# Kernel tuning notes

Measured on AMD Instinct MI355X. Metric: run time of the kernel, lower is better.

## Reference

```python
import jax, jax.numpy as jnp
import numpy as np

B, Q, C, G = 16, 2000, 80, 100
COST_CLASS, COST_BBOX, COST_GIOU = 2.0, 5.0, 2.0
ALPHA, GAMMA = 0.25, 2.0
OTA_K = 5
CENTER_RADIUS = 2.5
MAX_ITERS = 1000  # safety cap on the (normally rarely-entered) rescue while-loop


def cxcywh_to_xyxy(b):
    cx, cy, w, h = jnp.split(b, 4, axis=-1)
    return jnp.concatenate([cx - 0.5 * w, cy - 0.5 * h, cx + 0.5 * w, cy + 0.5 * h], -1)


def xyxy_to_cxcywh(b):
    x1, y1, x2, y2 = jnp.split(b, 4, axis=-1)
    return jnp.concatenate([(x1 + x2) * 0.5, (y1 + y2) * 0.5, x2 - x1, y2 - y1], -1)


def box_iou(a, b):
    # a: [Q,4], b: [G,4] xyxy -> iou [Q,G], union [Q,G]
    area_a = (a[:, 2] - a[:, 0]) * (a[:, 3] - a[:, 1])
    area_b = (b[:, 2] - b[:, 0]) * (b[:, 3] - b[:, 1])
    lt = jnp.maximum(a[:, None, :2], b[None, :, :2])
    rb = jnp.minimum(a[:, None, 2:], b[None, :, 2:])
    wh = jnp.clip(rb - lt, 0.0)
    inter = wh[..., 0] * wh[..., 1]
    union = area_a[:, None] + area_b[None, :] - inter
    return inter / union, union


def generalized_box_iou(a, b):
    iou, union = box_iou(a, b)
    lt = jnp.minimum(a[:, None, :2], b[None, :, :2])
    rb = jnp.maximum(a[:, None, 2:], b[None, :, 2:])
    wh = jnp.clip(rb - lt, 0.0)
    area = wh[..., 0] * wh[..., 1]
    return iou - (area - union) / area


def get_in_boxes_info(boxes_c, tgt_c):
    # boxes_c: [Q,4] cxcywh (abs), tgt_c: [G,4] cxcywh (abs)
    xy = cxcywh_to_xyxy(tgt_c)  # [G,4]
    ax = boxes_c[:, 0:1]  # [Q,1]
    ay = boxes_c[:, 1:2]
    in_box = (ax > xy[:, 0][None, :]) & (ax < xy[:, 2][None, :]) & \
             (ay > xy[:, 1][None, :]) & (ay < xy[:, 3][None, :])  # [Q,G]
    w = xy[:, 2] - xy[:, 0]
    h = xy[:, 3] - xy[:, 1]
    in_ctr = (ax > (tgt_c[:, 0] - CENTER_RADIUS * w)[None, :]) & \
             (ax < (tgt_c[:, 0] + CENTER_RADIUS * w)[None, :]) & \
             (ay > (tgt_c[:, 1] - CENTER_RADIUS * h)[None, :]) & \
             (ay < (tgt_c[:, 1] + CENTER_RADIUS * h)[None, :])
    fg_mask = in_box.any(1) | in_ctr.any(1)  # [Q]
    return fg_mask, in_box & in_ctr


def dynamic_k_matching(cost, ious):
    # cost, ious: [Q,G]
    topk_ious, _ = jax.lax.top_k(ious.T, OTA_K)  # [G,k]
    dyn_k = jnp.clip(topk_ious.sum(1).astype(jnp.int32), 1, None)  # [G], <= OTA_K
    # rank of each query within each gt column (ascending cost, stable ties)
    ranks = jnp.argsort(jnp.argsort(cost, axis=0), axis=0)
    M = (ranks < dyn_k[None, :]).astype(cost.dtype)  # topk(largest=False) per column

    onehot = lambda idx: jax.nn.one_hot(idx, G, dtype=cost.dtype)
    # resolve anchors matched to >1 gt: keep the min-cost gt
    conflict0 = M.sum(1) > 1  # stale mask reused inside the while loop (faithful to torch code)
    M = jnp.where(conflict0[:, None], onehot(jnp.argmin(cost, axis=1)), M)

    qidx = jnp.arange(Q)

    def cond(state):
        M, cost, it = state
        return ((M.sum(0) == 0).any()) & (it < MAX_ITERS)

    def body(state):
        M, cost, it = state
        matched = M.sum(1) > 0
        cost = cost + 100000.0 * matched[:, None].astype(cost.dtype)
        unmatched_gt = M.sum(0) == 0  # [G]
        pos = jnp.argmin(cost, axis=0)  # [G] best anchor per gt (same cost for all, as in torch)
        add = unmatched_gt[None, :] & (qidx[:, None] == pos[None, :])
        M = jnp.where(add, jnp.asarray(1.0, cost.dtype), M)
        has_conf = (M.sum(1) > 1).any()
        M = jnp.where((has_conf & conflict0)[:, None], onehot(jnp.argmin(cost, axis=1)), M)
        return M, cost, it + 1

    M, cost, _ = jax.lax.while_loop(cond, body, (M, cost, jnp.int32(0)))

    selected = M.sum(1) > 0  # [Q] bool
    gt_idx = jnp.argmax(M, axis=1).astype(jnp.int32)  # [Q] (valid where selected)
    cost_m = jnp.where(M == 0, jnp.asarray(1e30, cost.dtype), cost)
    matched_qid = jnp.argmin(cost_m, axis=0).astype(jnp.int32)  # [G]
    return selected, gt_idx, matched_qid, M


def _match_one(logits, boxes, gtb, labels, img):
    # logits [Q,C], boxes [Q,4] cxcywh, gtb [G,4] cxcywh norm, labels [G] int, img [4]
    prob = jax.nn.sigmoid(logits)
    boxes_abs = cxcywh_to_xyxy(boxes) * img
    gt_abs = cxcywh_to_xyxy(gtb) * img
    fg_mask, in_bc = get_in_boxes_info(xyxy_to_cxcywh(boxes_abs), xyxy_to_cxcywh(gt_abs))
    ious, _ = box_iou(boxes_abs, gt_abs)
    neg = (1.0 - ALPHA) * prob ** GAMMA * (-jnp.log(1.0 - prob + 1e-8))
    pos = ALPHA * (1.0 - prob) ** GAMMA * (-jnp.log(prob + 1e-8))
    cost_class = (pos - neg)[:, labels]  # [Q,G]
    cost_bbox = jnp.sum(jnp.abs(boxes_abs[:, None, :] / img - gt_abs[None, :, :] / img), -1)
    cost_giou = -generalized_box_iou(boxes_abs, gt_abs)
    cost = (COST_BBOX * cost_bbox + COST_CLASS * cost_class + COST_GIOU * cost_giou
            + 100.0 * (~in_bc).astype(cost_bbox.dtype)
            + 10000.0 * (~fg_mask)[:, None].astype(cost_bbox.dtype))
    return dynamic_k_matching(cost, ious)


def setup_inputs() -> dict:
    key = jax.random.key(0)
    k1, k2, k3, k4 = jax.random.split(key, 4)
    return {
        "pred_logits": jax.random.normal(k1, (B, Q, C), dtype=jnp.float32),
        "pred_boxes": jax.random.uniform(k2, (B, Q, 4), dtype=jnp.float32),
        "gt_boxes": jax.random.uniform(k3, (B, G, 4), dtype=jnp.float32),
        "labels": jax.random.randint(k4, (B, G), 0, C),
        "image_size_xyxy": jnp.ones((B, 4), dtype=jnp.float32),
    }


def reference(pred_logits, pred_boxes, gt_boxes, labels, image_size_xyxy):
    selected, gt_idx, matched_qid, M = jax.vmap(_match_one)(
        pred_logits, pred_boxes, gt_boxes, labels, image_size_xyxy)
    # selected [B,Q] bool, gt_idx [B,Q] int32, matched_qid [B,G] int32, M [B,Q,G] float
    return selected, gt_idx, matched_qid, M
```

## Files before the change

### kernel.cpp

```cpp
#include <hip/hip_runtime.h>
#include <stdint.h>

#define BATCH 16
#define NQ 2000
#define NC 80
#define NG 100
#define MAX_ITERS 1000
#define MAXC 96
#define QT 32
#define TILES 63
#define K1_TILEB (BATCH * TILES)
#define K1_BLOCKS (K1_TILEB + 400)
#define K3_BS 1024
#define NW3 16
#define NCAND 8
#define LSTRIDE 9
#define QINF 0x7fffffff
#define SQINF 0x7fff

#define OFF_SEL 0
#define OFF_GTI (BATCH * NQ)
#define OFF_MQ (2 * BATCH * NQ)
#define OFF_M (2 * BATCH * NQ + BATCH * NG)

#define WS_COST  0
#define WS_LISTS 12800000
#define WS_MW    12864000
#define WS_MIT   13376000
#define WS_CIDX  13440000
#define WS_CROW  13504000
#define WS_SCAL  14118400
#define WS_NEED  14118912

__device__ __forceinline__ float fmut(float c, int k) {
    for (int i = 0; i < k; ++i) c += 100000.0f;
    return c;
}

__device__ __forceinline__ bool lexlt(float v1, int i1, float v2, int i2) {
    return (v1 < v2) | ((v1 == v2) & (i1 < i2));
}

#define CE(vv, ii, a, b) do { \
    bool t_ = lexlt(vv[b], ii[b], vv[a], ii[a]); \
    float lo_ = t_ ? vv[b] : vv[a]; float hi_ = t_ ? vv[a] : vv[b]; \
    int loi_ = t_ ? ii[b] : ii[a]; int hii_ = t_ ? ii[a] : ii[b]; \
    vv[a] = lo_; vv[b] = hi_; ii[a] = loi_; ii[b] = hii_; \
} while (0)

#define INS8(vv, ii, val, idx) do { float v_ = (val); int i_ = (idx); \
    bool ins_ = lexlt(v_, i_, vv[7], ii[7]); \
    vv[7] = ins_ ? v_ : vv[7]; ii[7] = ins_ ? i_ : ii[7]; \
    CE(vv, ii, 6, 7); CE(vv, ii, 5, 6); CE(vv, ii, 4, 5); CE(vv, ii, 3, 4); \
    CE(vv, ii, 2, 3); CE(vv, ii, 1, 2); CE(vv, ii, 0, 1); \
} while (0)

#define MERGE8(va, ia) do { \
    for (int off_ = 1; off_ < 64; off_ <<= 1) { \
        float bv_[8]; int bi_[8]; \
        _Pragma("unroll") \
        for (int j_ = 0; j_ < 8; ++j_) { bv_[j_] = __shfl_xor(va[j_], off_, 64); bi_[j_] = __shfl_xor(ia[j_], off_, 64); } \
        float mv_[8]; int mi_[8]; \
        _Pragma("unroll") \
        for (int j_ = 0; j_ < 8; ++j_) { \
            bool t_ = lexlt(bv_[7 - j_], bi_[7 - j_], va[j_], ia[j_]); \
            mv_[j_] = t_ ? bv_[7 - j_] : va[j_]; mi_[j_] = t_ ? bi_[7 - j_] : ia[j_]; \
        } \
        _Pragma("unroll") \
        for (int d_ = 4; d_ >= 1; d_ >>= 1) { \
            _Pragma("unroll") \
            for (int i_ = 0; i_ < 8; ++i_) { \
                if ((i_ & d_) == 0) CE(mv_, mi_, i_, (i_ | d_)); \
            } \
        } \
        _Pragma("unroll") \
        for (int j_ = 0; j_ < 8; ++j_) { va[j_] = mv_[j_]; ia[j_] = mi_[j_]; } \
    } \
} while (0)

__device__ __forceinline__ void dynk_wave(int w, int lane,
                                          const float* __restrict__ pred_boxes,
                                          const float* __restrict__ gt_boxes,
                                          const float* __restrict__ img_sz,
                                          float* __restrict__ lists) {
    int b = w / NG, g = w - b * NG;
    const float i0 = img_sz[b * 4 + 0], i1 = img_sz[b * 4 + 1];
    const float i2 = img_sz[b * 4 + 2], i3 = img_sz[b * 4 + 3];
    const float4 gt = *reinterpret_cast<const float4*>(gt_boxes + (b * NG + g) * 4);
    float GX1 = (gt.x - 0.5f * gt.z) * i0, GY1 = (gt.y - 0.5f * gt.w) * i1;
    float GX2 = (gt.x + 0.5f * gt.z) * i2, GY2 = (gt.y + 0.5f * gt.w) * i3;
    float GA = (GX2 - GX1) * (GY2 - GY1);

    const float* pbox = pred_boxes + (size_t)b * NQ * 4;
    float tv[5]; int ti[5];
#pragma unroll
    for (int j = 0; j < 5; ++j) { tv[j] = INFINITY; ti[j] = QINF; }

    for (int q = lane; q < NQ; q += 64) {
        const float4 pb = *reinterpret_cast<const float4*>(pbox + q * 4);
        float x1 = (pb.x - 0.5f * pb.z) * i0, y1 = (pb.y - 0.5f * pb.w) * i1;
        float x2 = (pb.x + 0.5f * pb.z) * i2, y2 = (pb.y + 0.5f * pb.w) * i3;
        float aA = (x2 - x1) * (y2 - y1);
        float lx = fmaxf(x1, GX1), ly = fmaxf(y1, GY1);
        float rx = fminf(x2, GX2), ry = fminf(y2, GY2);
        float iw = fmaxf(rx - lx, 0.0f), ih = fmaxf(ry - ly, 0.0f);
        float inter = iw * ih;
        float uni = aA + GA - inter;
        float niou = -(inter / uni);
        bool ins = lexlt(niou, q, tv[4], ti[4]);
        tv[4] = ins ? niou : tv[4]; ti[4] = ins ? q : ti[4];
        CE(tv, ti, 3, 4); CE(tv, ti, 2, 3); CE(tv, ti, 1, 2); CE(tv, ti, 0, 1);
    }

#pragma unroll
    for (int off = 1; off < 64; off <<= 1) {
        float bv[5]; int bi[5];
#pragma unroll
        for (int j = 0; j < 5; ++j) { bv[j] = __shfl_xor(tv[j], off, 64); bi[j] = __shfl_xor(ti[j], off, 64); }
        float mv[8]; int mi[8];
#pragma unroll
        for (int j = 0; j < 3; ++j) { mv[j] = tv[j]; mi[j] = ti[j]; }
#pragma unroll
        for (int j = 3; j < 5; ++j) {
            bool t = lexlt(bv[7 - j], bi[7 - j], tv[j], ti[j]);
            mv[j] = t ? bv[7 - j] : tv[j]; mi[j] = t ? bi[7 - j] : ti[j];
        }
#pragma unroll
        for (int j = 5; j < 8; ++j) { mv[j] = bv[7 - j]; mi[j] = bi[7 - j]; }
#pragma unroll
        for (int d = 4; d >= 1; d >>= 1) {
#pragma unroll
            for (int i = 0; i < 8; ++i) {
                if ((i & d) == 0) CE(mv, mi, i, (i | d));
            }
        }
#pragma unroll
        for (int j = 0; j < 5; ++j) { tv[j] = mv[j]; ti[j] = mi[j]; }
    }

    if (lane == 0) {
        float s = -((((tv[0] + tv[1]) + tv[2]) + tv[3]) + tv[4]);
        int k = (int)s;
        if (k < 1) k = 1;
        lists[(size_t)w * LSTRIDE] = (float)k;
    }
}

__global__ __launch_bounds__(256) void fgcost_kernel(
    const float* __restrict__ logits, const float* __restrict__ pred_boxes,
    const float* __restrict__ gt_boxes, const int* __restrict__ labels,
    const float* __restrict__ img_sz, float* __restrict__ costT_all,
    float* __restrict__ rowamin, float* __restrict__ lists) {
    const int tid = threadIdx.x;

    if (blockIdx.x >= K1_TILEB) {
        int w = (blockIdx.x - K1_TILEB) * 4 + (tid >> 6);
        dynk_wave(w, tid & 63, pred_boxes, gt_boxes, img_sz, lists);
        return;
    }

    const int b = blockIdx.x / TILES;
    const int tile = blockIdx.x - b * TILES;
    const int q0 = tile * QT;

    __shared__ float ct[QT][NG + 1];
    __shared__ float s_rx1[NG], s_ry1[NG], s_rx2[NG], s_ry2[NG];
    __shared__ float s_clx[NG], s_chx[NG], s_cly[NG], s_chy[NG];
    __shared__ float s_gx1[NG], s_gy1[NG], s_gx2[NG], s_gy2[NG];
    __shared__ float s_d1[NG], s_d2[NG], s_d3[NG], s_d4[NG];
    __shared__ float s_ga[NG];
    __shared__ int s_lab[NG];
    __shared__ float pbx[QT][11];
    __shared__ unsigned fgm[QT];

    const float i0 = img_sz[b * 4 + 0], i1 = img_sz[b * 4 + 1];
    const float i2 = img_sz[b * 4 + 2], i3 = img_sz[b * 4 + 3];

    if (tid < NG) {
        const float4 gt = *reinterpret_cast<const float4*>(gt_boxes + (b * NG + tid) * 4);
        float GX1 = (gt.x - 0.5f * gt.z) * i0, GY1 = (gt.y - 0.5f * gt.w) * i1;
        float GX2 = (gt.x + 0.5f * gt.z) * i2, GY2 = (gt.y + 0.5f * gt.w) * i3;
        float tcx = (GX1 + GX2) * 0.5f, tcy = (GY1 + GY2) * 0.5f;
        float tw = GX2 - GX1, th = GY2 - GY1;
        float X1 = tcx - 0.5f * tw, Y1 = tcy - 0.5f * th;
        float X2 = tcx + 0.5f * tw, Y2 = tcy + 0.5f * th;
        float w_ = X2 - X1, h_ = Y2 - Y1;
        s_rx1[tid] = X1; s_ry1[tid] = Y1; s_rx2[tid] = X2; s_ry2[tid] = Y2;
        s_clx[tid] = tcx - 2.5f * w_; s_chx[tid] = tcx + 2.5f * w_;
        s_cly[tid] = tcy - 2.5f * h_; s_chy[tid] = tcy + 2.5f * h_;
        s_gx1[tid] = GX1; s_gy1[tid] = GY1; s_gx2[tid] = GX2; s_gy2[tid] = GY2;
        s_d1[tid] = GX1 / i0; s_d2[tid] = GY1 / i1; s_d3[tid] = GX2 / i2; s_d4[tid] = GY2 / i3;
        s_ga[tid] = (GX2 - GX1) * (GY2 - GY1);
        s_lab[tid] = labels[b * NG + tid];
    }
    if (tid < QT) {
        fgm[tid] = 0;
        int q = q0 + tid;
        if (q < NQ) {
            const float4 pb = *reinterpret_cast<const float4*>(pred_boxes + (size_t)(b * NQ + q) * 4);
            float x1 = (pb.x - 0.5f * pb.z) * i0, y1 = (pb.y - 0.5f * pb.w) * i1;
            float x2 = (pb.x + 0.5f * pb.z) * i2, y2 = (pb.y + 0.5f * pb.w) * i3;
            pbx[tid][0] = x1; pbx[tid][1] = y1; pbx[tid][2] = x2; pbx[tid][3] = y2;
            pbx[tid][4] = (x1 + x2) * 0.5f; pbx[tid][5] = (y1 + y2) * 0.5f;
            pbx[tid][6] = x1 / i0; pbx[tid][7] = y1 / i1; pbx[tid][8] = x2 / i2; pbx[tid][9] = y2 / i3;
            pbx[tid][10] = (x2 - x1) * (y2 - y1);
        }
    }
    __syncthreads();

    {
        int ql = tid & 31, part = tid >> 5;
        if (q0 + ql < NQ) {
            float ax = pbx[ql][4], ay = pbx[ql][5];
            int gbeg = part * 13;
            int gend = gbeg + 13 < NG ? gbeg + 13 : NG;
            bool any = false;
            for (int g = gbeg; g < gend; ++g) {
                bool in_box = (ax > s_rx1[g]) && (ax < s_rx2[g]) && (ay > s_ry1[g]) && (ay < s_ry2[g]);
                bool in_ctr = (ax > s_clx[g]) && (ax < s_chx[g]) && (ay > s_cly[g]) && (ay < s_chy[g]);
                any = any || in_box || in_ctr;
            }
            if (any) atomicOr(&fgm[ql], 1u);
        }
    }
    __syncthreads();

    for (int idx = tid; idx < QT * NG; idx += 256) {
        int ql = idx / NG, g = idx - ql * NG;
        int q = q0 + ql;
        if (q < NQ) {
            float x1 = pbx[ql][0], y1 = pbx[ql][1], x2 = pbx[ql][2], y2 = pbx[ql][3];
            float ax = pbx[ql][4], ay = pbx[ql][5];
            bool in_box = (ax > s_rx1[g]) && (ax < s_rx2[g]) && (ay > s_ry1[g]) && (ay < s_ry2[g]);
            bool in_ctr = (ax > s_clx[g]) && (ax < s_chx[g]) && (ay > s_cly[g]) && (ay < s_chy[g]);
            bool in_bc = in_box && in_ctr;
            bool fgb = fgm[ql] != 0;

            float lg = logits[(size_t)(b * NQ + q) * NC + s_lab[g]];
            float p = 1.0f / (1.0f + expf(-lg));
            float neg = 0.75f * (p * p) * (-logf(1.0f - p + 1e-8f));
            float pos = 0.25f * ((1.0f - p) * (1.0f - p)) * (-logf(p + 1e-8f));
            float cc = pos - neg;

            float cb = fabsf(pbx[ql][6] - s_d1[g]);
            cb = cb + fabsf(pbx[ql][7] - s_d2[g]);
            cb = cb + fabsf(pbx[ql][8] - s_d3[g]);
            cb = cb + fabsf(pbx[ql][9] - s_d4[g]);

            float aA = pbx[ql][10];
            float GX1 = s_gx1[g], GY1 = s_gy1[g], GX2 = s_gx2[g], GY2 = s_gy2[g];
            float lx = fmaxf(x1, GX1), ly = fmaxf(y1, GY1);
            float rx = fminf(x2, GX2), ry = fminf(y2, GY2);
            float iw = fmaxf(rx - lx, 0.0f), ih = fmaxf(ry - ly, 0.0f);
            float inter = iw * ih;
            float uni = aA + s_ga[g] - inter;
            float iou = inter / uni;
            float hx1 = fminf(x1, GX1), hy1 = fminf(y1, GY1);
            float hx2 = fmaxf(x2, GX2), hy2 = fmaxf(y2, GY2);
            float hw = fmaxf(hx2 - hx1, 0.0f), hh = fmaxf(hy2 - hy1, 0.0f);
            float harea = hw * hh;
            float giou = iou - (harea - uni) / harea;

            float cost = 5.0f * cb;
            cost = cost + 2.0f * cc;
            cost = cost + 2.0f * (-giou);
            cost = cost + (in_bc ? 0.0f : 100.0f);
            cost = cost + (fgb ? 0.0f : 10000.0f);
            ct[ql][g] = cost;
        }
    }
    __syncthreads();

    float* dst = costT_all + (size_t)b * NQ * NG;
    for (int idx = tid; idx < QT * NG; idx += 256) {
        int g = idx >> 5, ql = idx & 31;
        int q = q0 + ql;
        if (q < NQ) dst[(size_t)g * NQ + q] = ct[ql][g];
    }
    if (tid < QT && q0 + tid < NQ) {
        float mv = ct[tid][0]; int mg = 0;
        for (int g = 1; g < NG; ++g) { float v = ct[tid][g]; if (v < mv) { mv = v; mg = g; } }
        rowamin[b * NQ + q0 + tid] = (float)mg;
    }
}

__global__ __launch_bounds__(256) void init_kernel(const float* __restrict__ pred_boxes,
                                                   const float* __restrict__ gt_boxes,
                                                   const float* __restrict__ img_sz,
                                                   const float* __restrict__ costT_all,
                                                   float* __restrict__ lists) {
    const int tid = threadIdx.x;
    const int wid = tid >> 6, lane = tid & 63;

    if (blockIdx.x < 400) {
        int w = blockIdx.x * 4 + wid;
        int b = w / NG, g = w - b * NG;
        const float* col = costT_all + (size_t)b * NQ * NG + (size_t)g * NQ;

        float va[8]; int ia[8];
#pragma unroll
        for (int j = 0; j < 8; ++j) { va[j] = INFINITY; ia[j] = QINF; }
        for (int q = lane; q < NQ; q += 64) {
            float v = col[q];
            INS8(va, ia, v, q);
        }
        MERGE8(va, ia);
        if (lane == 0) {
            float* o = lists + (size_t)w * LSTRIDE;
            o[1] = (float)ia[0]; o[2] = (float)ia[1]; o[3] = (float)ia[2]; o[4] = (float)ia[3];
            o[5] = (float)ia[4]; o[6] = (float)ia[5]; o[7] = (float)ia[6]; o[8] = (float)ia[7];
        }
        return;
    }

    int w = (blockIdx.x - 400) * 4 + wid;
    dynk_wave(w, lane, pred_boxes, gt_boxes, img_sz, lists);
}

__global__ __launch_bounds__(K3_BS) void match_main(const float* __restrict__ lists,
                                                    const float* __restrict__ rowamin_all,
                                                    const float* __restrict__ costT_all,
                                                    char* __restrict__ ws) {
    const int b = blockIdx.x;
    const int tid = threadIdx.x;
    const int wave = tid >> 6;
    const int lane = tid & 63;

    __shared__ uint32_t Mw[4][NQ];
    __shared__ float crow[MAXC][NG + 1];
    __shared__ int m_it[NQ];
    __shared__ int16_t c16[NQ];
    __shared__ int16_t cand[NG][NCAND];
    __shared__ int crowq[MAXC];
    __shared__ int colcnt[NG];
    __shared__ int needscan[NG];
    __shared__ int touched[128];
    __shared__ int nconf0, nscan, ntq, persist;

    uint32_t* MwG = (uint32_t*)(ws + WS_MW) + (size_t)b * 4 * NQ;
    int16_t* mitG = (int16_t*)(ws + WS_MIT) + (size_t)b * NQ;
    int16_t* cidxG = (int16_t*)(ws + WS_CIDX) + (size_t)b * NQ;
    float* crowG = (float*)(ws + WS_CROW) + (size_t)b * MAXC * NG;
    int* scalG = (int*)(ws + WS_SCAL) + b * 8;
    const float* costT = costT_all + (size_t)b * NQ * NG;
    const float* rowamin_b = rowamin_all + b * NQ;

    if (tid == 0) { nconf0 = 0; nscan = 0; ntq = 0; persist = 0; }
    for (int q = tid; q < NQ; q += K3_BS) {
        Mw[0][q] = 0; Mw[1][q] = 0; Mw[2][q] = 0; Mw[3][q] = 0;
        c16[q] = -1; m_it[q] = QINF;
    }
    __syncthreads();

    if (tid < NG) {
        const float* o = lists + (size_t)(b * NG + tid) * LSTRIDE;
        int k = (int)o[0];
        int word = tid >> 5;
        uint32_t bit = 1u << (tid & 31);
        for (int j = 0; j < NCAND; ++j) {
            float f = o[1 + j];
            cand[tid][j] = (f >= 32767.0f) ? (int16_t)SQINF : (int16_t)(int)f;
        }
        for (int j = 0; j < 5; ++j)
            if (j < k) atomicOr(&Mw[word][(int)o[1 + j]], bit);
        colcnt[tid] = k;
    }
    __syncthreads();

    for (int q = tid; q < NQ; q += K3_BS) {
        uint32_t w0 = Mw[0][q], w1 = Mw[1][q], w2 = Mw[2][q], w3 = Mw[3][q];
        int pc = __popc(w0) + __popc(w1) + __popc(w2) + __popc(w3);
        if (pc > 1) {
            int slot = atomicAdd(&nconf0, 1);
            int c = (slot < MAXC) ? slot : -1;
            c16[q] = (c >= 0) ? (int16_t)c : (int16_t)-2;
            m_it[q] = -1;
            if (c >= 0) crowq[c] = q;
            int mg = (int)rowamin_b[q];
            uint32_t words[4] = {w0, w1, w2, w3};
            for (int w = 0; w < 4; ++w) {
                uint32_t word = words[w];
                while (word) {
                    int bp = __ffs(word) - 1;
                    word &= word - 1;
                    atomicSub(&colcnt[w * 32 + bp], 1);
                }
                Mw[w][q] = 0;
            }
            Mw[mg >> 5][q] = 1u << (mg & 31);
            atomicAdd(&colcnt[mg], 1);
        } else if (pc == 1) {
            m_it[q] = -1;
        }
    }
    __syncthreads();

    const int nc0 = nconf0;
    const int ncached = (nc0 < MAXC) ? nc0 : MAXC;
    const bool hasOvf = nc0 > MAXC;
    for (int i = tid; i < ncached * NG; i += K3_BS) {
        int c = i / NG, g = i - c * NG;
        crow[c][g] = costT[(size_t)g * NQ + crowq[c]];
    }
    __syncthreads();

    int unm = __syncthreads_or(tid < NG && colcnt[tid] == 0);
    int L = 0;

    for (int it = 0; it < MAX_ITERS; ++it) {
        if (!unm) break;
        L = it + 1;

        for (int i = tid; i < ncached * NG; i += K3_BS) {
            int c = i / NG, g = i - c * NG;
            crow[c][g] += 100000.0f;
        }
        if (tid < NG && colcnt[tid] == 0) {
            int g = tid;
            int win = -1;
            for (int j = 0; j < NCAND; ++j) {
                int qi = cand[g][j];
                if (qi != SQINF && m_it[qi] >= it) { win = qi; break; }
            }
            if (win >= 0) {
                atomicOr(&Mw[g >> 5][win], 1u << (g & 31));
                atomicMin(&m_it[win], it);
                colcnt[g] = 1;
                touched[atomicAdd(&ntq, 1)] = win;
            } else {
                needscan[atomicAdd(&nscan, 1)] = g;
            }
        }
        __syncthreads();

        int ns = nscan;
        if (ns > 0) {
            for (int s = wave; s < ns; s += NW3) {
                int g = needscan[s];
                const float* col = costT + (size_t)g * NQ;
                float mv = INFINITY; int mi = QINF;
                for (int q = lane; q < NQ; q += 64) {
                    if (m_it[q] >= it) {
                        float v = col[q];
                        if (v < mv || (v == mv && q < mi)) { mv = v; mi = q; }
                    }
                }
                for (int off = 1; off < 64; off <<= 1) {
                    float ov = __shfl_xor(mv, off); int oi = __shfl_xor(mi, off);
                    if (ov < mv || (ov == mv && oi < mi)) { mv = ov; mi = oi; }
                }
                if (mi == QINF) {
                    for (int q = lane; q < NQ; q += 64) {
                        int nq = it - m_it[q]; if (nq < 0) nq = 0;
                        float v = fmut(col[q], nq);
                        if (v < mv || (v == mv && q < mi)) { mv = v; mi = q; }
                    }
                    for (int off = 1; off < 64; off <<= 1) {
                        float ov = __shfl_xor(mv, off); int oi = __shfl_xor(mi, off);
                        if (ov < mv || (ov == mv && oi < mi)) { mv = ov; mi = oi; }
                    }
                }
                if (lane == 0) {
                    atomicOr(&Mw[g >> 5][mi], 1u << (g & 31));
                    atomicMin(&m_it[mi], it);
                    colcnt[g] = 1;
                    touched[atomicAdd(&ntq, 1)] = mi;
                }
            }
            __syncthreads();
        }

        int myconf = (tid == 0 && persist) ? 1 : 0;
        int nt = ntq;
        for (int s = tid; s < nt; s += K3_BS) {
            int q = touched[s];
            int pc = __popc(Mw[0][q]) + __popc(Mw[1][q]) + __popc(Mw[2][q]) + __popc(Mw[3][q]);
            if (pc > 1) {
                myconf = 1;
                if (c16[q] == -1) persist = 1;
            }
        }
        int hc = __syncthreads_or(myconf);
        if (!hc) break;

        if (tid == 0) { ntq = 0; nscan = 0; }
        for (int c = tid; c < ncached; c += K3_BS) {
            int q = crowq[c];
            float mv = crow[c][0]; int mg = 0;
            for (int g = 1; g < NG; ++g) { float v = crow[c][g]; if (v < mv) { mv = v; mg = g; } }
            int keepw = mg >> 5;
            uint32_t keepb = 1u << (mg & 31);
            for (int w = 0; w < 4; ++w) {
                uint32_t word = Mw[w][q];
                uint32_t keep = (w == keepw) ? keepb : 0u;
                uint32_t toclear = word & ~keep;
                while (toclear) {
                    int bp = __ffs(toclear) - 1;
                    toclear &= toclear - 1;
                    atomicSub(&colcnt[w * 32 + bp], 1);
                }
                if (keep && !(word & keep)) atomicAdd(&colcnt[mg], 1);
                Mw[w][q] = keep;
            }
        }
        if (hasOvf) {
            for (int q = tid; q < NQ; q += K3_BS) {
                if (c16[q] != -2) continue;
                int k = it + 1;
                float mv = fmut(costT[q], k); int mg = 0;
                for (int g = 1; g < NG; ++g) {
                    float v = fmut(costT[(size_t)g * NQ + q], k);
                    if (v < mv) { mv = v; mg = g; }
                }
                int keepw = mg >> 5;
                uint32_t keepb = 1u << (mg & 31);
                for (int w = 0; w < 4; ++w) {
                    uint32_t word = Mw[w][q];
                    uint32_t keep = (w == keepw) ? keepb : 0u;
                    uint32_t toclear = word & ~keep;
                    while (toclear) {
                        int bp = __ffs(toclear) - 1;
                        toclear &= toclear - 1;
                        atomicSub(&colcnt[w * 32 + bp], 1);
                    }
                    if (keep && !(word & keep)) atomicAdd(&colcnt[mg], 1);
                    Mw[w][q] = keep;
                }
            }
        }
        __syncthreads();
        unm = __syncthreads_or(tid < NG && colcnt[tid] == 0);
    }

    uint32_t* MwF = &Mw[0][0];
    for (int i = tid; i < 4 * NQ; i += K3_BS) MwG[i] = MwF[i];
    for (int q = tid; q < NQ; q += K3_BS) {
        int v = m_it[q];
        mitG[q] = (v > 32000) ? (int16_t)SQINF : (int16_t)v;
        cidxG[q] = c16[q];
    }
    for (int i = tid; i < ncached * NG; i += K3_BS) crowG[i] = crow[i / NG][i - (i / NG) * NG];
    if (tid == 0) { scalG[0] = nc0; scalG[1] = L; }
}

__global__ __launch_bounds__(256) void finish_ex(const char* __restrict__ ws,
                                                 const float* __restrict__ costT_all,
                                                 float* __restrict__ out) {
    const int tid = threadIdx.x;
    const int blk = blockIdx.x;

    if (blk < 400) {
        int w = blk * 4 + (tid >> 6);
        int lane = tid & 63;
        int b = w / NG, g = w - b * NG;
        const int* scalG = (const int*)(ws + WS_SCAL) + b * 8;
        const int L = scalG[1];
        const uint32_t* MwP = (const uint32_t*)(ws + WS_MW) + (size_t)b * 4 * NQ + (size_t)(g >> 5) * NQ;
        const int16_t* mitG = (const int16_t*)(ws + WS_MIT) + (size_t)b * NQ;
        const int16_t* cidxG = (const int16_t*)(ws + WS_CIDX) + (size_t)b * NQ;
        const float* crowG = (const float*)(ws + WS_CROW) + (size_t)b * MAXC * NG;
        const float* col = costT_all + (size_t)b * NQ * NG + (size_t)g * NQ;
        const uint32_t bit = 1u << (g & 31);

        float mv = INFINITY; int mi = QINF;
        for (int q = lane; q < NQ; q += 64) {
            float v = 1e30f;
            if (MwP[q] & bit) {
                int c = cidxG[q];
                if (c >= 0) v = crowG[c * NG + g];
                else {
                    int m = mitG[q];
                    int nq = (m == SQINF) ? 0 : (L - 1 - m);
                    if (nq < 0) nq = 0;
                    v = fmut(col[q], nq);
                }
            }
            if (v < mv || (v == mv && q < mi)) { mv = v; mi = q; }
        }
        for (int off = 1; off < 64; off <<= 1) {
            float ov = __shfl_xor(mv, off); int oi = __shfl_xor(mi, off);
            if (ov < mv || (ov == mv && oi < mi)) { mv = ov; mi = oi; }
        }
        if (lane == 0) out[OFF_MQ + b * NG + g] = (float)mi;
        return;
    }

    if (blk < 525) {
        int idx = (blk - 400) * 256 + tid;
        if (idx < BATCH * NQ) {
            int b = idx / NQ, q = idx - b * NQ;
            const uint32_t* MwG = (const uint32_t*)(ws + WS_MW) + (size_t)b * 4 * NQ;
            uint32_t w0 = MwG[q], w1 = MwG[NQ + q], w2 = MwG[2 * NQ + q], w3 = MwG[3 * NQ + q];
            out[OFF_SEL + idx] = (w0 | w1 | w2 | w3) ? 1.0f : 0.0f;
            int gi = 0;
            if (w0) gi = __ffs(w0) - 1;
            else if (w1) gi = 32 + __ffs(w1) - 1;
            else if (w2) gi = 64 + __ffs(w2) - 1;
            else if (w3) gi = 96 + __ffs(w3) - 1;
            out[OFF_GTI + idx] = (float)gi;
        }
        return;
    }

    const int e = blk - 525;
    const int b = e >> 3, j = e & 7;
    const int q0 = j * 250;
    __shared__ uint32_t msk[4][256];
    const uint32_t* MwG = (const uint32_t*)(ws + WS_MW) + (size_t)b * 4 * NQ;
    for (int i = tid; i < 1000; i += 256) {
        int w = i / 250, q = i - w * 250;
        msk[w][q] = MwG[w * NQ + q0 + q];
    }
    __syncthreads();
    float4* dst = reinterpret_cast<float4*>(out + OFF_M + (size_t)b * NQ * NG + (size_t)q0 * NG);
    for (int i = tid; i < 6250; i += 256) {
        int flat = i * 4;
        int ql = flat / NG;
        int g0 = flat - ql * NG;
        uint32_t w = msk[g0 >> 5][ql];
        int sh = g0 & 31;
        float4 v;
        v.x = ((w >> sh) & 1) ? 1.0f : 0.0f;
        v.y = ((w >> (sh + 1)) & 1) ? 1.0f : 0.0f;
        v.z = ((w >> (sh + 2)) & 1) ? 1.0f : 0.0f;
        v.w = ((w >> (sh + 3)) & 1) ? 1.0f : 0.0f;
        dst[i] = v;
    }
}

__global__ __launch_bounds__(K3_BS) void match_mono(const float* __restrict__ lists,
                                                    float* __restrict__ out) {
    const int b = blockIdx.x;
    const int tid = threadIdx.x;
    const int wave = tid >> 6;
    const int lane = tid & 63;

    __shared__ uint32_t Msh[NQ][4];
    __shared__ float crow[MAXC][NG + 1];
    __shared__ int m_it[NQ];
    __shared__ int16_t cidx[NQ];
    __shared__ int candq[NG][NCAND];
    __shared__ int crowq[MAXC];
    __shared__ int colcnt[NG];
    __shared__ int needscan[NG];
    __shared__ int touched[128];
    __shared__ int nconf0, nscan, ntq, persist;

    float* costT = out + OFF_M + (size_t)b * NQ * NG;
    float* selOut = out + OFF_SEL + b * NQ;
    float* gtiOut = out + OFF_GTI + b * NQ;
    const float* rowamin_b = out + OFF_GTI + b * NQ;
    float* mqOut = out + OFF_MQ + b * NG;

    if (tid == 0) { nconf0 = 0; nscan = 0; ntq = 0; persist = 0; }
    for (int q = tid; q < NQ; q += K3_BS) {
        Msh[q][0] = 0; Msh[q][1] = 0; Msh[q][2] = 0; Msh[q][3] = 0;
        cidx[q] = -1; m_it[q] = QINF;
    }
    __syncthreads();
    if (tid < NG) {
        const float* o = lists + (size_t)(b * NG + tid) * LSTRIDE;
        int k = (int)o[0];
        int word = tid >> 5;
        uint32_t bit = 1u << (tid & 31);
        for (int j = 0; j < NCAND; ++j) candq[tid][j] = (int)o[1 + j];
        for (int j = 0; j < 5; ++j)
            if (j < k) atomicOr(&Msh[candq[tid][j]][word], bit);
        colcnt[tid] = k;
    }
    __syncthreads();
    for (int q = tid; q < NQ; q += K3_BS) {
        uint4 m = *reinterpret_cast<const uint4*>(&Msh[q][0]);
        int pc = __popc(m.x) + __popc(m.y) + __popc(m.z) + __popc(m.w);
        if (pc > 1) {
            int slot = atomicAdd(&nconf0, 1);
            int c = (slot < MAXC) ? slot : -1;
            cidx[q] = (c >= 0) ? (int16_t)c : (int16_t)-2;
            m_it[q] = -1;
            if (c >= 0) crowq[c] = q;
            int mg = (int)rowamin_b[q];
            uint32_t words[4] = {m.x, m.y, m.z, m.w};
            for (int w = 0; w < 4; ++w) {
                uint32_t word = words[w];
                while (word) {
                    int bp = __ffs(word) - 1;
                    word &= word - 1;
                    atomicSub(&colcnt[w * 32 + bp], 1);
                }
                Msh[q][w] = 0;
            }
            Msh[q][mg >> 5] = 1u << (mg & 31);
            atomicAdd(&colcnt[mg], 1);
        } else if (pc == 1) {
            m_it[q] = -1;
        }
    }
    __syncthreads();
    const int ncached = (nconf0 < MAXC) ? nconf0 : MAXC;
    const bool hasOvf = nconf0 > MAXC;
    for (int i = tid; i < ncached * NG; i += K3_BS) {
        int c = i / NG, g = i - c * NG;
        crow[c][g] = costT[(size_t)g * NQ + crowq[c]];
    }
    __syncthreads();
    int unm = __syncthreads_or(tid < NG && colcnt[tid] == 0);
    int L = 0;
    for (int it = 0; it < MAX_ITERS; ++it) {
        if (!unm) break;
        L = it + 1;
        for (int i = tid; i < ncached * NG; i += K3_BS) {
            int c = i / NG, g = i - c * NG;
            crow[c][g] += 100000.0f;
        }
        if (tid < NG && colcnt[tid] == 0) {
            int g = tid;
            int win = -1;
            for (int j = 0; j < NCAND; ++j) {
                int qi = candq[g][j];
                if (qi != QINF && m_it[qi] >= it) { win = qi; break; }
            }
            if (win >= 0) {
                atomicOr(&Msh[win][g >> 5], 1u << (g & 31));
                atomicMin(&m_it[win], it);
                colcnt[g] = 1;
                touched[atomicAdd(&ntq, 1)] = win;
            } else {
                needscan[atomicAdd(&nscan, 1)] = g;
            }
        }
        __syncthreads();
        int ns = nscan;
        if (ns > 0) {
            for (int s = wave; s < ns; s += NW3) {
                int g = needscan[s];
                const float* col = costT + (size_t)g * NQ;
                float mv = INFINITY; int mi = QINF;
                for (int q = lane; q < NQ; q += 64) {
                    if (m_it[q] >= it) {
                        float v = col[q];
                        if (v < mv || (v == mv && q < mi)) { mv = v; mi = q; }
                    }
                }
                for (int off = 1; off < 64; off <<= 1) {
                    float ov = __shfl_xor(mv, off); int oi = __shfl_xor(mi, off);
                    if (ov < mv || (ov == mv && oi < mi)) { mv = ov; mi = oi; }
                }
                if (mi == QINF) {
                    for (int q = lane; q < NQ; q += 64) {
                        int nq = it - m_it[q]; if (nq < 0) nq = 0;
                        float v = fmut(col[q], nq);
                        if (v < mv || (v == mv && q < mi)) { mv = v; mi = q; }
                    }
                    for (int off = 1; off < 64; off <<= 1) {
                        float ov = __shfl_xor(mv, off); int oi = __shfl_xor(mi, off);
                        if (ov < mv || (ov == mv && oi < mi)) { mv = ov; mi = oi; }
                    }
                }
                if (lane == 0) {
                    atomicOr(&Msh[mi][g >> 5], 1u << (g & 31));
                    atomicMin(&m_it[mi], it);
                    colcnt[g] = 1;
                    touched[atomicAdd(&ntq, 1)] = mi;
                }
            }
            __syncthreads();
        }
        int myconf = (tid == 0 && persist) ? 1 : 0;
        int nt = ntq;
        for (int s = tid; s < nt; s += K3_BS) {
            int q = touched[s];
            uint4 m = *reinterpret_cast<const uint4*>(&Msh[q][0]);
            int pc = __popc(m.x) + __popc(m.y) + __popc(m.z) + __popc(m.w);
            if (pc > 1) {
                myconf = 1;
                if (cidx[q] == -1) persist = 1;
            }
        }
        int hc = __syncthreads_or(myconf);
        if (!hc) break;
        if (tid == 0) { ntq = 0; nscan = 0; }
        for (int c = tid; c < ncached; c += K3_BS) {
            int q = crowq[c];
            float mv = crow[c][0]; int mg = 0;
            for (int g = 1; g < NG; ++g) { float v = crow[c][g]; if (v < mv) { mv = v; mg = g; } }
            int keepw = mg >> 5;
            uint32_t keepb = 1u << (mg & 31);
            for (int w = 0; w < 4; ++w) {
                uint32_t word = Msh[q][w];
                uint32_t keep = (w == keepw) ? keepb : 0u;
                uint32_t toclear = word & ~keep;
                while (toclear) {
                    int bp = __ffs(toclear) - 1;
                    toclear &= toclear - 1;
                    atomicSub(&colcnt[w * 32 + bp], 1);
                }
                if (keep && !(word & keep)) atomicAdd(&colcnt[mg], 1);
                Msh[q][w] = keep;
            }
        }
        if (hasOvf) {
            for (int q = tid; q < NQ; q += K3_BS) {
                if (cidx[q] != -2) continue;
                int k = it + 1;
                float mv = fmut(costT[q], k); int mg = 0;
                for (int g = 1; g < NG; ++g) {
                    float v = fmut(costT[(size_t)g * NQ + q], k);
                    if (v < mv) { mv = v; mg = g; }
                }
                int keepw = mg >> 5;
                uint32_t keepb = 1u << (mg & 31);
                for (int w = 0; w < 4; ++w) {
                    uint32_t word = Msh[q][w];
                    uint32_t keep = (w == keepw) ? keepb : 0u;
                    uint32_t toclear = word & ~keep;
                    while (toclear) {
                        int bp = __ffs(toclear) - 1;
                        toclear &= toclear - 1;
                        atomicSub(&colcnt[w * 32 + bp], 1);
                    }
                    if (keep && !(word & keep)) atomicAdd(&colcnt[mg], 1);
                    Msh[q][w] = keep;
                }
            }
        }
        __syncthreads();
        unm = __syncthreads_or(tid < NG && colcnt[tid] == 0);
    }
    for (int g = wave; g < NG; g += NW3) {
        int word = g >> 5;
        uint32_t bit = 1u << (g & 31);
        const float* col = costT + (size_t)g * NQ;
        float mv = INFINITY; int mi = QINF;
        for (int q = lane; q < NQ; q += 64) {
            float v = 1e30f;
            if (Msh[q][word] & bit) {
                int c = cidx[q];
                if (c >= 0) v = crow[c][g];
                else {
                    int nq = L - 1 - m_it[q]; if (nq < 0) nq = 0;
                    v = fmut(col[q], nq);
                }
            }
            if (v < mv || (v == mv && q < mi)) { mv = v; mi = q; }
        }
        for (int off = 1; off < 64; off <<= 1) {
            float ov = __shfl_xor(mv, off); int oi = __shfl_xor(mi, off);
            if (ov < mv || (ov == mv && oi < mi)) { mv = ov; mi = oi; }
        }
        if (lane == 0) mqOut[g] = (float)mi;
    }
    for (int q = tid; q < NQ; q += K3_BS) {
        uint4 m = *reinterpret_cast<const uint4*>(&Msh[q][0]);
        selOut[q] = (m.x | m.y | m.z | m.w) ? 1.0f : 0.0f;
        int gi = 0;
        if (m.x) gi = __ffs(m.x) - 1;
        else if (m.y) gi = 32 + __ffs(m.y) - 1;
        else if (m.z) gi = 64 + __ffs(m.z) - 1;
        else if (m.w) gi = 96 + __ffs(m.w) - 1;
        gtiOut[q] = (float)gi;
    }
    __syncthreads();
    for (int i = tid; i < NQ * NG; i += K3_BS) {
        int q = i / NG;
        int g = i - q * NG;
        costT[i] = (Msh[q][g >> 5] & (1u << (g & 31))) ? 1.0f : 0.0f;
    }
}

extern "C" void kernel_launch(void* const* d_in, const int* in_sizes, int n_in,
                              void* d_out, int out_size, void* d_ws, size_t ws_size,
                              hipStream_t stream) {
    const float* logits = (const float*)d_in[0];
    const float* pboxes = (const float*)d_in[1];
    const float* gboxes = (const float*)d_in[2];
    const int* labels = (const int*)d_in[3];
    const float* img = (const float*)d_in[4];
    float* out = (float*)d_out;
    char* ws = (char*)d_ws;

    if (ws_size >= (size_t)WS_NEED) {
        float* costT = (float*)(ws + WS_COST);
        float* lists = (float*)(ws + WS_LISTS);
        fgcost_kernel<<<K1_BLOCKS, 256, 0, stream>>>(logits, pboxes, gboxes, labels, img,
                                                     costT, out + OFF_GTI, lists);
        init_kernel<<<400, 256, 0, stream>>>(pboxes, gboxes, img, costT, lists);
        match_main<<<BATCH, K3_BS, 0, stream>>>(lists, out + OFF_GTI, costT, ws);
        finish_ex<<<653, 256, 0, stream>>>(ws, costT, out);
    } else {
        float* lists = (float*)ws;
        fgcost_kernel<<<K1_TILEB, 256, 0, stream>>>(logits, pboxes, gboxes, labels, img,
                                                    out + OFF_M, out + OFF_GTI, lists);
        init_kernel<<<800, 256, 0, stream>>>(pboxes, gboxes, img, out + OFF_M, lists);
        match_mono<<<BATCH, K3_BS, 0, stream>>>(lists, out);
    }
}
```

Baseline: 84.45 us.

## Fuse per-column top-8 candidate selection into cost kernel, drop init kernel

The cost kernel now computes, for each gt column, a per-tile top-8 of (cost, query) pairs from its shared-memory cost tile and writes them to a new workspace region. The matching kernel merges the 63 tile partials per column itself, so the separate init_kernel launch and its full re-read of the transposed cost matrix are removed. This saves one launch and a large global read, but it adds per-tile insertion work and partial-list writes to the cost kernel, adds a merge stage in the low-parallelism matching kernel, and needs a larger workspace.

```diff
diff --git a/kernel.cpp b/kernel.cpp
--- a/kernel.cpp
+++ b/kernel.cpp
@@ -25,12 +25,13 @@
 
 #define WS_COST  0
 #define WS_LISTS 12800000
-#define WS_MW    12864000
-#define WS_MIT   13376000
-#define WS_CIDX  13440000
-#define WS_CROW  13504000
-#define WS_SCAL  14118400
-#define WS_NEED  14118912
+#define WS_CAND8 12857600
+#define WS_MW    19308800
+#define WS_MIT   19820800
+#define WS_CIDX  19884800
+#define WS_CROW  19948800
+#define WS_SCAL  20563200
+#define WS_NEED  20563712
 
 __device__ __forceinline__ float fmut(float c, int k) {
     for (int i = 0; i < k; ++i) c += 100000.0f;
@@ -150,7 +151,8 @@
     const float* __restrict__ logits, const float* __restrict__ pred_boxes,
     const float* __restrict__ gt_boxes, const int* __restrict__ labels,
     const float* __restrict__ img_sz, float* __restrict__ costT_all,
-    float* __restrict__ rowamin, float* __restrict__ lists) {
+    float* __restrict__ rowamin, float* __restrict__ lists,
+    float2* __restrict__ cand8) {
     const int tid = threadIdx.x;
 
     if (blockIdx.x >= K1_TILEB) {
@@ -282,6 +284,22 @@
         for (int g = 1; g < NG; ++g) { float v = ct[tid][g]; if (v < mv) { mv = v; mg = g; } }
         rowamin[b * NQ + q0 + tid] = (float)mg;
     }
+    if (cand8 != nullptr && tid < NG) {
+        int g = tid;
+        float va[8]; int ia[8];
+#pragma unroll
+        for (int j = 0; j < 8; ++j) { va[j] = INFINITY; ia[j] = QINF; }
+        for (int ql = 0; ql < QT; ++ql) {
+            int q = q0 + ql;
+            float v = (q < NQ) ? ct[ql][g] : INFINITY;
+            int qi = (q < NQ) ? q : QINF;
+            INS8(va, ia, v, qi);
+        }
+        float2* o = cand8 + ((size_t)(b * NG + g) * TILES + tile) * 8;
+#pragma unroll
+        for (int j = 0; j < 8; ++j)
+            o[j] = make_float2(va[j], (ia[j] == QINF) ? 3.0e9f : (float)ia[j]);
+    }
 }
 
 __global__ __launch_bounds__(256) void init_kernel(const float* __restrict__ pred_boxes,
@@ -342,6 +360,7 @@
     int16_t* cidxG = (int16_t*)(ws + WS_CIDX) + (size_t)b * NQ;
     float* crowG = (float*)(ws + WS_CROW) + (size_t)b * MAXC * NG;
     int* scalG = (int*)(ws + WS_SCAL) + b * 8;
+    const float2* cand8 = (const float2*)(ws + WS_CAND8);
     const float* costT = costT_all + (size_t)b * NQ * NG;
     const float* rowamin_b = rowamin_all + b * NQ;
 
@@ -352,17 +371,31 @@
     }
     __syncthreads();
 
+    for (int g = wave; g < NG; g += NW3) {
+        const float2* cnd = cand8 + (size_t)(b * NG + g) * TILES * 8;
+        float va[8]; int ia[8];
+#pragma unroll
+        for (int j = 0; j < 8; ++j) { va[j] = INFINITY; ia[j] = QINF; }
+        for (int i = lane; i < TILES * 8; i += 64) {
+            float2 p = cnd[i];
+            int qi = (p.y > 2.0e9f) ? QINF : (int)p.y;
+            INS8(va, ia, p.x, qi);
+        }
+        MERGE8(va, ia);
+        if (lane == 0) {
+#pragma unroll
+            for (int j = 0; j < NCAND; ++j)
+                cand[g][j] = (ia[j] >= 32767) ? (int16_t)SQINF : (int16_t)ia[j];
+        }
+    }
+    __syncthreads();
+
     if (tid < NG) {
-        const float* o = lists + (size_t)(b * NG + tid) * LSTRIDE;
-        int k = (int)o[0];
+        int k = (int)lists[(size_t)(b * NG + tid) * LSTRIDE];
         int word = tid >> 5;
         uint32_t bit = 1u << (tid & 31);
-        for (int j = 0; j < NCAND; ++j) {
-            float f = o[1 + j];
-            cand[tid][j] = (f >= 32767.0f) ? (int16_t)SQINF : (int16_t)(int)f;
-        }
         for (int j = 0; j < 5; ++j)
-            if (j < k) atomicOr(&Mw[word][(int)o[1 + j]], bit);
+            if (j < k) atomicOr(&Mw[word][(int)cand[tid][j]], bit);
         colcnt[tid] = k;
     }
     __syncthreads();
@@ -881,15 +914,15 @@
     if (ws_size >= (size_t)WS_NEED) {
         float* costT = (float*)(ws + WS_COST);
         float* lists = (float*)(ws + WS_LISTS);
+        float2* cand8 = (float2*)(ws + WS_CAND8);
         fgcost_kernel<<<K1_BLOCKS, 256, 0, stream>>>(logits, pboxes, gboxes, labels, img,
-                                                     costT, out + OFF_GTI, lists);
-        init_kernel<<<400, 256, 0, stream>>>(pboxes, gboxes, img, costT, lists);
+                                                     costT, out + OFF_GTI, lists, cand8);
         match_main<<<BATCH, K3_BS, 0, stream>>>(lists, out + OFF_GTI, costT, ws);
         finish_ex<<<653, 256, 0, stream>>>(ws, costT, out);
     } else {
         float* lists = (float*)ws;
         fgcost_kernel<<<K1_TILEB, 256, 0, stream>>>(logits, pboxes, gboxes, labels, img,
-                                                    out + OFF_M, out + OFF_GTI, lists);
+                                                    out + OFF_M, out + OFF_GTI, lists, nullptr);
         init_kernel<<<800, 256, 0, stream>>>(pboxes, gboxes, img, out + OFF_M, lists);
         match_mono<<<BATCH, K3_BS, 0, stream>>>(lists, out);
     }
```

Measured after the change: 133.7 us. 1.58x slower.
